# Kernel tuning notes

Hardware: AMD Instinct MI355X
Metric: run time of the kernel (lower is better)

Reference implementation:

```python
import jax, jax.numpy as jnp
import numpy as np

N_HEADS = 16


def setup_inputs() -> dict:
    key = jax.random.key(0)
    ks = jax.random.split(key, 9)
    B, S, D = 2, 2048, 1024
    s = 0.02
    return {
        "x": jax.random.normal(ks[0], (B, S, D), dtype=jnp.float32),
        "Wq": jax.random.normal(ks[1], (D, D), dtype=jnp.float32) * s,
        "bq": jax.random.normal(ks[2], (D,), dtype=jnp.float32) * s,
        "Wk": jax.random.normal(ks[3], (D, D), dtype=jnp.float32) * s,
        "bk": jax.random.normal(ks[4], (D,), dtype=jnp.float32) * s,
        "Wv": jax.random.normal(ks[5], (D, D), dtype=jnp.float32) * s,
        "bv": jax.random.normal(ks[6], (D,), dtype=jnp.float32) * s,
        "Wo": jax.random.normal(ks[7], (D, D), dtype=jnp.float32) * s,
        "bo": jax.random.normal(ks[8], (D,), dtype=jnp.float32) * s,
    }


def reference(x, Wq, bq, Wk, bk, Wv, bv, Wo, bo):
    B, S, D = x.shape
    H = N_HEADS
    hd = D // H
    # projections -> [B, H, S, hd]
    def heads(w, b):
        return (x @ w + b).reshape(B, S, H, hd).transpose(0, 2, 1, 3)
    Q, K, V = heads(Wq, bq), heads(Wk, bk), heads(Wv, bv)
    scores = jnp.einsum("bhqd,bhkd->bhqk", Q, K)
    causal = jnp.triu(jnp.ones((S, S), dtype=bool), k=1)  # True above diagonal
    scores = jnp.where(causal, -jnp.inf, scores)
    w = jax.nn.softmax(scores / jnp.sqrt(jnp.float32(hd)), axis=-1)
    ctx = jnp.einsum("bhqk,bhkd->bhqd", w, V).transpose(0, 2, 1, 3).reshape(B, S, D)
    return ctx @ Wo + bo
```

## Files before the change

kernel.cpp:

```cpp
#include <hip/hip_runtime.h>
#include <hip/hip_bf16.h>

typedef __attribute__((ext_vector_type(8))) short short8;
typedef __attribute__((ext_vector_type(4))) float floatx4;
typedef __attribute__((ext_vector_type(4))) int intx4;
typedef __attribute__((ext_vector_type(2))) int intx2;

#define D_MODEL 1024
#define SEQ     2048
#define NB      2
#define NH      16
#define HD      64
#define MROWS   4096
#define CZ      (0.125f * 1.44269504f)

__device__ __forceinline__ floatx4 mfma_bf16(short8 a, short8 b, floatx4 c) {
  return __builtin_amdgcn_mfma_f32_16x16x32_bf16(a, b, c, 0, 0, 0);
}

__device__ __forceinline__ void dma16(const __hip_bfloat16* g, __hip_bfloat16* l) {
  __builtin_amdgcn_global_load_lds(
      (const __attribute__((address_space(1))) void*)g,
      (__attribute__((address_space(3))) void*)l, 16, 0, 0);
}
#define WAIT_VM(n)  __asm__ __volatile__("s_waitcnt vmcnt(" #n ")" ::: "memory")
#define BARRIER()   __asm__ __volatile__("s_barrier" ::: "memory")
#define WAIT_LGKM() __asm__ __volatile__("s_waitcnt lgkmcnt(0)" ::: "memory")

__device__ __forceinline__ int pack2bf(float a, float b) {
  unsigned ua = __builtin_bit_cast(unsigned, a) + 0x8000u;
  unsigned ub = __builtin_bit_cast(unsigned, b) + 0x8000u;
  return (int)__builtin_amdgcn_perm(ub, ua, 0x07060302u);
}

__device__ __forceinline__ int cvtpk(float a, float b) {
  int r;
  __asm__("v_cvt_pk_bf16_f32 %0, %1, %2" : "=v"(r) : "v"(a), "v"(b));
  return r;
}

__global__ void prep_kernel(const float* __restrict__ x, __hip_bfloat16* __restrict__ xb,
                            const float* __restrict__ W0, const float* __restrict__ W1,
                            const float* __restrict__ W2, const float* __restrict__ W3,
                            __hip_bfloat16* __restrict__ T0, __hip_bfloat16* __restrict__ T1,
                            __hip_bfloat16* __restrict__ T2, __hip_bfloat16* __restrict__ T3) {
  const int z = blockIdx.z;
  if (z == 4) {
    const int tid = threadIdx.y * 32 + threadIdx.x;
    const int base = ((blockIdx.y * 32 + blockIdx.x) * 256 + tid) * 16;
#pragma unroll
    for (int c = 0; c < 4; c++) {
      float4 v = *(const float4*)(x + base + c * 4);
      __hip_bfloat16 tmp[4];
      tmp[0] = __float2bfloat16(v.x);
      tmp[1] = __float2bfloat16(v.y);
      tmp[2] = __float2bfloat16(v.z);
      tmp[3] = __float2bfloat16(v.w);
      *(ushort4*)(xb + base + c * 4) = *(ushort4*)tmp;
    }
    return;
  }
  const float* W = (z == 0) ? W0 : (z == 1) ? W1 : (z == 2) ? W2 : W3;
  __hip_bfloat16* Wt = (z == 0) ? T0 : (z == 1) ? T1 : (z == 2) ? T2 : T3;
  __shared__ float tile[32][33];
  int k0 = blockIdx.x * 32, n0 = blockIdx.y * 32;
  int tx = threadIdx.x, ty = threadIdx.y;
#pragma unroll
  for (int i = 0; i < 4; i++)
    tile[ty + 8 * i][tx] = W[(size_t)(k0 + ty + 8 * i) * D_MODEL + n0 + tx];
  __syncthreads();
#pragma unroll
  for (int i = 0; i < 4; i++)
    Wt[(size_t)(n0 + ty + 8 * i) * D_MODEL + k0 + tx] = __float2bfloat16(tile[tx][ty + 8 * i]);
}

template <int MODE>
__global__ __launch_bounds__(256) void gemm_kernel(
    const __hip_bfloat16* __restrict__ X,
    const __hip_bfloat16* __restrict__ Wt0, const __hip_bfloat16* __restrict__ Wt1,
    const __hip_bfloat16* __restrict__ Wt2,
    const float* __restrict__ b0, const float* __restrict__ b1, const float* __restrict__ b2,
    void* __restrict__ out0, void* __restrict__ out1, void* __restrict__ out2) {
  constexpr int MT = (MODE == 0) ? 128 : 64;
  constexpr int I = MT / 32;
  constexpr int NKT = D_MODEL / 32;
  constexpr int STAGE_BYTES = 3 * (MT * 32 + 128 * 32) * 2;
  constexpr int EPI_BYTES = 64 * 132 * 4;
  constexpr int SMEM_BYTES = (STAGE_BYTES > EPI_BYTES) ? STAGE_BYTES : EPI_BYTES;

  int n_idx, z, m_idx;
  if constexpr (MODE == 0) {
    const int lin = blockIdx.x + 8 * (blockIdx.y + 3 * blockIdx.z);
    n_idx = lin / 96;
    const int rem = lin - n_idx * 96;
    z = rem >> 5;
    m_idx = rem & 31;
  } else {
    const int lin = blockIdx.x + 8 * blockIdx.z;
    n_idx = lin >> 6;
    z = 0;
    m_idx = lin & 63;
  }

  const __hip_bfloat16* Wt = (z == 0) ? Wt0 : (z == 1) ? Wt1 : Wt2;
  const float* bias = (z == 0) ? b0 : (z == 1) ? b1 : b2;
  void* outp = (z == 0) ? out0 : (z == 1) ? out1 : out2;
  const float scale = (MODE == 0 && z == 0) ? CZ : 1.f;

  __shared__ __attribute__((aligned(16))) char smem[SMEM_BYTES];
  __hip_bfloat16* As = (__hip_bfloat16*)smem;
  __hip_bfloat16* Bs = (__hip_bfloat16*)smem + 3 * MT * 32;
  float* Es = (float*)smem;

  const int n0 = n_idx * 128;
  const int m0 = m_idx * MT;
  const int t = threadIdx.x;
  const int lane = t & 63, w = t >> 6;
  const int wm = (w >> 1) * (MT / 2), wn = (w & 1) * 64;
  const int lr = lane & 15;
  const int lq = lane >> 4;

  const __hip_bfloat16* Xp = X + (size_t)m0 * D_MODEL;
  const __hip_bfloat16* Wp = Wt + (size_t)n0 * D_MODEL;

  const int lrow = lane >> 2;
  const int skg = (((lane & 3) ^ ((lane >> 3) & 3)) << 3);
  const int srowA = ((MT == 128) ? (w << 5) : (w << 4)) + lrow;
  const int sbA0 = (((MT == 128) ? (w << 5) : (w << 4)) << 5);
  const int sbA1 = sbA0 + (16 << 5);
  const int srowB = (w << 5) + lrow;
  const int sbB0 = ((w << 5) << 5);
  const int sbB1 = sbB0 + (16 << 5);

#define STAGE_G(kt_, buf_)                                                              \
  {                                                                                     \
    const int kn_ = (kt_) * 32;                                                         \
    __hip_bfloat16* A_ = As + (buf_) * (MT * 32);                                       \
    __hip_bfloat16* B_ = Bs + (buf_) * (128 * 32);                                      \
    dma16(Xp + (size_t)srowA * D_MODEL + kn_ + skg, A_ + sbA0);                         \
    if (MT == 128) dma16(Xp + (size_t)(srowA + 16) * D_MODEL + kn_ + skg, A_ + sbA1);   \
    dma16(Wp + (size_t)srowB * D_MODEL + kn_ + skg, B_ + sbB0);                         \
    dma16(Wp + (size_t)(srowB + 16) * D_MODEL + kn_ + skg, B_ + sbB1);                  \
  }

  floatx4 acc[I][4];
#pragma unroll
  for (int i = 0; i < I; i++)
#pragma unroll
    for (int j = 0; j < 4; j++) acc[i][j] = (floatx4){0.f, 0.f, 0.f, 0.f};

  STAGE_G(0, 0);
  STAGE_G(1, 1);

  const int rcol = ((lq ^ ((lr >> 1) & 3)) << 3);

  int cb = 0;
  for (int kt = 0; kt < NKT; kt++) {
    if (kt < NKT - 1) {
      if constexpr (MODE == 0) WAIT_VM(4);
      else                     WAIT_VM(3);
    } else {
      WAIT_VM(0);
    }
    BARRIER();
    if (kt + 2 < NKT) {
      const int nb = (cb == 0) ? 2 : cb - 1;
      STAGE_G(kt + 2, nb);
    }
    const __hip_bfloat16* Ac = As + cb * (MT * 32);
    const __hip_bfloat16* Bc = Bs + cb * (128 * 32);
    short8 af[I], bfr[4];
#pragma unroll
    for (int i = 0; i < I; i++) af[i] = *(const short8*)&Ac[(wm + i * 16 + lr) * 32 + rcol];
#pragma unroll
    for (int j = 0; j < 4; j++) bfr[j] = *(const short8*)&Bc[(wn + j * 16 + lr) * 32 + rcol];
#pragma unroll
    for (int i = 0; i < I; i++)
#pragma unroll
      for (int j = 0; j < 4; j++) acc[i][j] = mfma_bf16(af[i], bfr[j], acc[i][j]);
    cb = (cb == 2) ? 0 : cb + 1;
  }
#undef STAGE_G

  float bvj[4];
#pragma unroll
  for (int j = 0; j < 4; j++) bvj[j] = bias[n0 + wn + j * 16 + lr];

  if constexpr (MODE == 1) {
    BARRIER();
#pragma unroll
    for (int i = 0; i < I; i++) {
      const int rowb = wm + i * 16 + lq * 4;
#pragma unroll
      for (int j = 0; j < 4; j++)
#pragma unroll
        for (int r = 0; r < 4; r++)
          Es[(rowb + r) * 132 + wn + j * 16 + lr] = acc[i][j][r] + bvj[j];
    }
    WAIT_LGKM();
    BARRIER();
    const int L = t >> 2, nseg = (t & 3) * 32;
    float* op = (float*)outp + (size_t)(m0 + L) * D_MODEL + n0 + nseg;
    const float* src = &Es[L * 132 + nseg];
#pragma unroll
    for (int k = 0; k < 8; k++) *(float4*)(op + 4 * k) = *(const float4*)(src + 4 * k);
  } else if (z != 2) {
    for (int c = 0; c < 2; c++) {
      BARRIER();
#pragma unroll
      for (int i2 = 0; i2 < 2; i2++) {
        const int i = 2 * c + i2;
        const int rowb = (w >> 1) * 32 + i2 * 16 + lq * 4;
#pragma unroll
        for (int j = 0; j < 4; j++)
#pragma unroll
          for (int r = 0; r < 4; r++)
            Es[(rowb + r) * 132 + wn + j * 16 + lr] = (acc[i][j][r] + bvj[j]) * scale;
      }
      WAIT_LGKM();
      BARRIER();
      const int L = t >> 2, nseg = (t & 3) * 32;
      const int m = m0 + ((L >> 5) << 6) + (c << 5) + (L & 31);
      const int bb = m >> 11, s = m & 2047;
      const int nn = n0 + nseg;
      __hip_bfloat16* op = (__hip_bfloat16*)outp +
          (((size_t)(bb * NH + (nn >> 6)) * SEQ + s) * HD + (nn & 63));
      const float* src = &Es[L * 132 + nseg];
#pragma unroll
      for (int k = 0; k < 4; k++) {
        intx4 pk;
        pk[0] = pack2bf(src[8 * k + 0], src[8 * k + 1]);
        pk[1] = pack2bf(src[8 * k + 2], src[8 * k + 3]);
        pk[2] = pack2bf(src[8 * k + 4], src[8 * k + 5]);
        pk[3] = pack2bf(src[8 * k + 6], src[8 * k + 7]);
        *(intx4*)(op + 8 * k) = pk;
      }
    }
  } else {
    for (int c = 0; c < 2; c++) {
      BARRIER();
#pragma unroll
      for (int j2 = 0; j2 < 2; j2++) {
        const int j = 2 * c + j2;
        const int nl = ((w & 1) << 5) + (j2 << 4) + lr;
#pragma unroll
        for (int i = 0; i < I; i++) {
          const int moff = (w >> 1) * 64 + i * 16 + lq * 4;
          floatx4 v = acc[i][j];
          v[0] += bvj[j]; v[1] += bvj[j]; v[2] += bvj[j]; v[3] += bvj[j];
          *(floatx4*)&Es[nl * 132 + moff] = v;
        }
      }
      WAIT_LGKM();
      BARRIER();
      const int nl = t >> 2, mseg = (t & 3) * 32;
      const int n = n0 + ((nl >> 5) << 6) + (c << 5) + (nl & 31);
      const int s0 = m0 & 2047, bb = m0 >> 11;
      __hip_bfloat16* op = (__hip_bfloat16*)outp +
          (((size_t)(bb * NH + (n >> 6)) * HD + (n & 63)) * SEQ + s0 + mseg);
      const float* src = &Es[nl * 132 + mseg];
#pragma unroll
      for (int k = 0; k < 4; k++) {
        intx4 pk;
        pk[0] = pack2bf(src[8 * k + 0], src[8 * k + 1]);
        pk[1] = pack2bf(src[8 * k + 2], src[8 * k + 3]);
        pk[2] = pack2bf(src[8 * k + 4], src[8 * k + 5]);
        pk[3] = pack2bf(src[8 * k + 6], src[8 * k + 7]);
        *(intx4*)(op + 8 * k) = pk;
      }
    }
  }
}

__global__ __launch_bounds__(256, 4) void attn_kernel(
    const __hip_bfloat16* __restrict__ Q, const __hip_bfloat16* __restrict__ Kg,
    const __hip_bfloat16* __restrict__ Vt, __hip_bfloat16* __restrict__ ctx) {
  const int bh = blockIdx.x;
  const int b = bh >> 4, h = bh & 15;
  const int qt = 31 - blockIdx.y;
  const int t = threadIdx.x, lane = t & 63, w = t >> 6;
  const int lr = lane & 15, lq = lane >> 4;
  const int wr = w & 1, wb = w >> 1;

  __shared__ __attribute__((aligned(16))) __hip_bfloat16 Ks[2][64 * 64];
  __shared__ __attribute__((aligned(16))) __hip_bfloat16 VTs[2][64 * 64];

  const __hip_bfloat16* Qb = Q + (size_t)bh * SEQ * HD;
  const __hip_bfloat16* Kb = Kg + (size_t)bh * SEQ * HD;
  const __hip_bfloat16* Vb = Vt + (size_t)bh * HD * SEQ;

  const int qrow0 = qt * 64 + wr * 32;

  short8 qf[2][2];
#pragma unroll
  for (int rt = 0; rt < 2; rt++)
#pragma unroll
    for (int ks = 0; ks < 2; ks++)
      qf[rt][ks] = *(const short8*)(Qb + (size_t)(qrow0 + rt * 16 + lr) * HD + ks * 32 + lq * 8);

  const int srow = (w << 4) + (lane >> 3);
  const int sgl = lane & 7;
  const int sb0 = (w << 4) << 6;
  const int sb1 = ((w << 4) + 8) << 6;

#define STAGE(tb, nb)                                                                  \
  {                                                                                    \
    const int r0 = srow, r1 = srow + 8;                                                \
    dma16(Kb + ((size_t)((tb) + r0) << 6) + ((sgl ^ (r0 & 7)) << 3), &Ks[nb][sb0]);    \
    dma16(Kb + ((size_t)((tb) + r1) << 6) + ((sgl ^ (r1 & 7)) << 3), &Ks[nb][sb1]);    \
    dma16(Vb + (size_t)r0 * SEQ + (tb) + ((sgl ^ (r0 & 7)) << 3), &VTs[nb][sb0]);      \
    dma16(Vb + (size_t)r1 * SEQ + (tb) + ((sgl ^ (r1 & 7)) << 3), &VTs[nb][sb1]);      \
  }

  const int nkt = qt + 1;
  STAGE(0, 0);

  floatx4 o[2][4];
#pragma unroll
  for (int rt = 0; rt < 2; rt++)
#pragma unroll
    for (int dt = 0; dt < 4; dt++) o[rt][dt] = (floatx4){0.f, 0.f, 0.f, 0.f};
  floatx4 lsacc[2];
  lsacc[0] = (floatx4){0.f, 0.f, 0.f, 0.f};
  lsacc[1] = (floatx4){0.f, 0.f, 0.f, 0.f};

  short8 ones;
#pragma unroll
  for (int j = 0; j < 8; j++) ones[j] = (short)0x3F80;

  const int kfb0 = ((wb << 4) + lr) << 6;
  const int kg0 = ((lq ^ (lr & 7)) << 3);
  const int kg1 = (((4 + lq) ^ (lr & 7)) << 3);
  const int vga = (((wb * 2 + (lq >> 1)) ^ (lr & 7)) << 3) + ((lq & 1) << 2);
  const int vgb = (((4 + wb * 2 + (lq >> 1)) ^ (lr & 7)) << 3) + ((lq & 1) << 2);

  for (int kt = 0; kt < nkt; kt++) {
    WAIT_VM(0);
    BARRIER();
    if (kt + 1 < nkt) STAGE((kt + 1) << 6, (kt + 1) & 1);

    const int kw0 = (kt << 6) + (wb << 4);
    if (kw0 <= qrow0 + 31) {
      const __hip_bfloat16* Kc = Ks[kt & 1];
      const __hip_bfloat16* Vc = VTs[kt & 1];

      short8 kf[2][2];
#pragma unroll
      for (int nt = 0; nt < 2; nt++) {
        kf[0][nt] = *(const short8*)&Kc[(nt << 11) + kfb0 + kg0];
        kf[1][nt] = *(const short8*)&Kc[(nt << 11) + kfb0 + kg1];
      }
      floatx4 s[2][2];
#pragma unroll
      for (int rt = 0; rt < 2; rt++)
#pragma unroll
        for (int nt = 0; nt < 2; nt++) s[rt][nt] = (floatx4){0.f, 0.f, 0.f, 0.f};
#pragma unroll
      for (int ks = 0; ks < 2; ks++)
#pragma unroll
        for (int nt = 0; nt < 2; nt++) {
          s[0][nt] = mfma_bf16(kf[ks][nt], qf[0][ks], s[0][nt]);
          s[1][nt] = mfma_bf16(kf[ks][nt], qf[1][ks], s[1][nt]);
        }

      const bool need_mask = (kw0 + 47 > qrow0);
      short8 pf[2];
#pragma unroll
      for (int rt = 0; rt < 2; rt++) {
        const int q = qrow0 + rt * 16 + lr;
        intx4 pk;
#pragma unroll
        for (int nt = 0; nt < 2; nt++) {
          const int kbase = (kt << 6) + (nt << 5) + (wb << 4) + (lq << 2);
          float x0 = s[rt][nt][0], x1 = s[rt][nt][1], x2 = s[rt][nt][2], x3 = s[rt][nt][3];
          if (need_mask) {
            x0 = (kbase + 0 <= q) ? x0 : -1e30f;
            x1 = (kbase + 1 <= q) ? x1 : -1e30f;
            x2 = (kbase + 2 <= q) ? x2 : -1e30f;
            x3 = (kbase + 3 <= q) ? x3 : -1e30f;
          }
          const float p0 = __builtin_amdgcn_exp2f(x0);
          const float p1 = __builtin_amdgcn_exp2f(x1);
          const float p2 = __builtin_amdgcn_exp2f(x2);
          const float p3 = __builtin_amdgcn_exp2f(x3);
          pk[2 * nt + 0] = cvtpk(p0, p1);
          pk[2 * nt + 1] = cvtpk(p2, p3);
        }
        pf[rt] = __builtin_bit_cast(short8, pk);
      }

      lsacc[0] = mfma_bf16(ones, pf[0], lsacc[0]);
      lsacc[1] = mfma_bf16(ones, pf[1], lsacc[1]);

#pragma unroll
      for (int dt = 0; dt < 4; dt++) {
        const int rb = ((dt << 4) + lr) << 6;
        intx4 vi;
        *(intx2*)&vi = *(const intx2*)&Vc[rb + vga];
        *(((intx2*)&vi) + 1) = *(const intx2*)&Vc[rb + vgb];
        short8 vf = __builtin_bit_cast(short8, vi);
        o[0][dt] = mfma_bf16(vf, pf[0], o[0][dt]);
        o[1][dt] = mfma_bf16(vf, pf[1], o[1][dt]);
      }
    }
  }

  BARRIER();
  if (wb == 1) {
    float* d0 = (float*)&Ks[0][0];
    float* d1 = (float*)&Ks[1][0];
    float* dl = (float*)&VTs[0][0];
    const int base = (wr << 10) + (lane << 4);
#pragma unroll
    for (int dt = 0; dt < 4; dt++) *(floatx4*)&d0[base + (dt << 2)] = o[0][dt];
#pragma unroll
    for (int dt = 0; dt < 4; dt++) *(floatx4*)&d1[base + (dt << 2)] = o[1][dt];
    dl[(wr << 7) + (lane << 1)] = lsacc[0][0];
    dl[(wr << 7) + (lane << 1) + 1] = lsacc[1][0];
    WAIT_LGKM();
  }
  BARRIER();
  if (wb == 0) {
    const float* d0 = (const float*)&Ks[0][0];
    const float* d1 = (const float*)&Ks[1][0];
    const float* dl = (const float*)&VTs[0][0];
    const int base = (wr << 10) + (lane << 4);
#pragma unroll
    for (int dt = 0; dt < 4; dt++) {
      o[0][dt] += *(const floatx4*)&d0[base + (dt << 2)];
      o[1][dt] += *(const floatx4*)&d1[base + (dt << 2)];
    }
    float inv[2];
    inv[0] = 1.f / (lsacc[0][0] + dl[(wr << 7) + (lane << 1)]);
    inv[1] = 1.f / (lsacc[1][0] + dl[(wr << 7) + (lane << 1) + 1]);
#pragma unroll
    for (int rt = 0; rt < 2; rt++) {
      const int row = qrow0 + rt * 16 + lr;
      __hip_bfloat16* cp = ctx + (size_t)b * SEQ * D_MODEL + (size_t)row * D_MODEL + h * HD;
#pragma unroll
      for (int dt = 0; dt < 4; dt++) {
        ushort4 pk;
        __hip_bfloat16* pp = (__hip_bfloat16*)&pk;
#pragma unroll
        for (int r = 0; r < 4; r++) pp[r] = __float2bfloat16(o[rt][dt][r] * inv[rt]);
        *(ushort4*)(cp + (dt << 4) + (lq << 2)) = pk;
      }
    }
  }
#undef STAGE
}

extern "C" void kernel_launch(void* const* d_in, const int* in_sizes, int n_in,
                              void* d_out, int out_size, void* d_ws, size_t ws_size,
                              hipStream_t stream) {
  const float* x  = (const float*)d_in[0];
  const float* Wq = (const float*)d_in[1];
  const float* bq = (const float*)d_in[2];
  const float* Wk = (const float*)d_in[3];
  const float* bk = (const float*)d_in[4];
  const float* Wv = (const float*)d_in[5];
  const float* bv = (const float*)d_in[6];
  const float* Wo = (const float*)d_in[7];
  const float* bo = (const float*)d_in[8];

  char* ws = (char*)d_ws;
  const size_t MB = 1u << 20;
  __hip_bfloat16* xb  = (__hip_bfloat16*)(ws + 0 * MB);
  __hip_bfloat16* wtq = (__hip_bfloat16*)(ws + 8 * MB);
  __hip_bfloat16* wtk = (__hip_bfloat16*)(ws + 10 * MB);
  __hip_bfloat16* wtv = (__hip_bfloat16*)(ws + 12 * MB);
  __hip_bfloat16* wto = (__hip_bfloat16*)(ws + 14 * MB);
  __hip_bfloat16* qb  = (__hip_bfloat16*)(ws + 16 * MB);
  __hip_bfloat16* kb  = (__hip_bfloat16*)(ws + 24 * MB);
  __hip_bfloat16* vt  = (__hip_bfloat16*)(ws + 32 * MB);
  __hip_bfloat16* ctx = xb;

  prep_kernel<<<dim3(32, 32, 5), dim3(32, 8), 0, stream>>>(x, xb, Wq, Wk, Wv, Wo,
                                                           wtq, wtk, wtv, wto);
  gemm_kernel<0><<<dim3(8, 3, 32), 256, 0, stream>>>(xb, wtq, wtk, wtv, bq, bk, bv,
                                                     (void*)qb, (void*)kb, (void*)vt);
  attn_kernel<<<dim3(32, 32), 256, 0, stream>>>(qb, kb, vt, ctx);
  gemm_kernel<1><<<dim3(8, 1, 64), 256, 0, stream>>>(ctx, wto, wto, wto, bo, bo, bo,
                                                     d_out, d_out, d_out);
}
```

Before: 188.0 us.

## Replace QKV projection GEMM with 256x256-tile, 512-thread double-buffered kernel

Adds a new QKV projection kernel that computes 256x256 output tiles with 8 waves, K-step 64, XOR-swizzled LDS, and double-buffered global-to-LDS DMA. Each load is split into quarters so the next tile's loads interleave with MFMA work, and s_setprio is raised around the MFMA blocks. The goal is more data reuse per loaded byte and fewer blocks than the 128x128 tiles. The trade-off is 128KB of LDS, only 192 blocks (fewer than the CU count), and more barriers per K step. The old MODE 0 code is removed from the templated GEMM, which now serves only the output projection.

Result: no change. 186.6 us (-0.7%).

```diff
diff --git a/kernel.cpp b/kernel.cpp
--- a/kernel.cpp
+++ b/kernel.cpp
@@ -72,6 +72,195 @@
 #pragma unroll
   for (int i = 0; i < 4; i++)
     Wt[(size_t)(n0 + ty + 8 * i) * D_MODEL + k0 + tx] = __float2bfloat16(tile[tx][ty + 8 * i]);
+}
+
+__global__ __launch_bounds__(512, 2) void gemm256_kernel(
+    const __hip_bfloat16* __restrict__ X,
+    const __hip_bfloat16* __restrict__ Wt0, const __hip_bfloat16* __restrict__ Wt1,
+    const __hip_bfloat16* __restrict__ Wt2,
+    const float* __restrict__ b0, const float* __restrict__ b1, const float* __restrict__ b2,
+    void* __restrict__ out0, void* __restrict__ out1, void* __restrict__ out2) {
+  constexpr int NKT = D_MODEL / 64;
+  constexpr int BUFE = 256 * 64;
+
+  const int z = blockIdx.y;
+  const __hip_bfloat16* Wt = (z == 0) ? Wt0 : (z == 1) ? Wt1 : Wt2;
+  const float* bias = (z == 0) ? b0 : (z == 1) ? b1 : b2;
+  void* outp = (z == 0) ? out0 : (z == 1) ? out1 : out2;
+  const float scale = (z == 0) ? CZ : 1.f;
+
+  __shared__ __attribute__((aligned(16))) char smem[131072];
+  __hip_bfloat16* As = (__hip_bfloat16*)smem;
+  __hip_bfloat16* Bs = (__hip_bfloat16*)smem + 2 * BUFE;
+  float* Es = (float*)smem;
+
+  const int n0 = blockIdx.x * 256;
+  const int m0 = blockIdx.z * 256;
+  const int t = threadIdx.x;
+  const int lane = t & 63, w = t >> 6;
+  const int wm = w >> 2, wn = w & 3;
+  const int lr = lane & 15, lq = lane >> 4;
+
+  const __hip_bfloat16* Xp = X + (size_t)m0 * D_MODEL;
+  const __hip_bfloat16* Wp = Wt + (size_t)n0 * D_MODEL;
+
+  const int srow = t >> 3;
+  const int sg = (t & 7) ^ (srow & 7);
+  const int wbase = (w << 3) << 6;
+
+#define STAGE_A8(kt_, u_)                                                             \
+  dma16(Xp + (size_t)(((u_) << 6) + srow) * D_MODEL + ((kt_) << 6) + (sg << 3),       \
+        As + (((kt_) & 1) ? BUFE : 0) + ((u_) << 12) + wbase)
+#define STAGE_B8(kt_, u_)                                                             \
+  dma16(Wp + (size_t)(((u_) << 6) + srow) * D_MODEL + ((kt_) << 6) + (sg << 3),       \
+        Bs + (((kt_) & 1) ? BUFE : 0) + ((u_) << 12) + wbase)
+
+  floatx4 acc[8][4];
+#pragma unroll
+  for (int i = 0; i < 8; i++)
+#pragma unroll
+    for (int j = 0; j < 4; j++) acc[i][j] = (floatx4){0.f, 0.f, 0.f, 0.f};
+
+  STAGE_B8(0, 0); STAGE_B8(0, 1); STAGE_B8(0, 2); STAGE_B8(0, 3);
+  STAGE_A8(0, 0); STAGE_A8(0, 2); STAGE_A8(0, 1); STAGE_A8(0, 3);
+
+#define READ_A2(dst, IB)                                                              \
+  _Pragma("unroll") for (int i2 = 0; i2 < 2; i2++) {                                  \
+    const int ra = (wm << 7) + (((IB) + i2) << 4) + lr;                               \
+    _Pragma("unroll") for (int ks = 0; ks < 2; ks++)                                  \
+      dst[i2][ks] = *(const short8*)&Ac[(ra << 6) + ((((ks << 2) + lq) ^ (ra & 7)) << 3)]; \
+  }
+#define MFMA_Q(IB, afr)                                                               \
+  __builtin_amdgcn_s_setprio(1);                                                      \
+  _Pragma("unroll") for (int i2 = 0; i2 < 2; i2++)                                    \
+  _Pragma("unroll") for (int j = 0; j < 4; j++) {                                     \
+    acc[(IB) + i2][j] = mfma_bf16(afr[i2][0], bf[j][0], acc[(IB) + i2][j]);           \
+    acc[(IB) + i2][j] = mfma_bf16(afr[i2][1], bf[j][1], acc[(IB) + i2][j]);           \
+  }                                                                                   \
+  __builtin_amdgcn_s_setprio(0);
+
+  for (int kt = 0; kt < NKT; kt++) {
+    const __hip_bfloat16* Ac = As + ((kt & 1) ? BUFE : 0);
+    const __hip_bfloat16* Bc = Bs + ((kt & 1) ? BUFE : 0);
+    const bool pre = (kt + 1 < NKT);
+
+    WAIT_VM(2);
+    BARRIER();
+    if (pre) { STAGE_B8(kt + 1, 0); STAGE_B8(kt + 1, 1); }
+    short8 bf[4][2];
+#pragma unroll
+    for (int j = 0; j < 4; j++) {
+      const int rb = (wn << 6) + (j << 4) + lr;
+#pragma unroll
+      for (int ks = 0; ks < 2; ks++)
+        bf[j][ks] = *(const short8*)&Bc[(rb << 6) + ((((ks << 2) + lq) ^ (rb & 7)) << 3)];
+    }
+    {
+      short8 a0[2][2];
+      READ_A2(a0, 0);
+      MFMA_Q(0, a0);
+    }
+    BARRIER();
+
+    if (pre) { STAGE_B8(kt + 1, 2); STAGE_B8(kt + 1, 3); }
+    {
+      short8 a1[2][2];
+      READ_A2(a1, 2);
+      MFMA_Q(2, a1);
+    }
+    BARRIER();
+
+    if (pre) { WAIT_VM(4); } else { WAIT_VM(0); }
+    BARRIER();
+    if (pre) { STAGE_A8(kt + 1, 0); STAGE_A8(kt + 1, 2); }
+    {
+      short8 a2[2][2];
+      READ_A2(a2, 4);
+      MFMA_Q(4, a2);
+    }
+    BARRIER();
+
+    if (pre) { STAGE_A8(kt + 1, 1); STAGE_A8(kt + 1, 3); }
+    {
+      short8 a3[2][2];
+      READ_A2(a3, 6);
+      MFMA_Q(6, a3);
+    }
+    BARRIER();
+  }
+#undef READ_A2
+#undef MFMA_Q
+#undef STAGE_A8
+#undef STAGE_B8
+
+  float bvj[4];
+#pragma unroll
+  for (int j = 0; j < 4; j++) bvj[j] = bias[n0 + (wn << 6) + j * 16 + lr];
+
+  if (z != 2) {
+    for (int c = 0; c < 4; c++) {
+      BARRIER();
+#pragma unroll
+      for (int i2 = 0; i2 < 2; i2++) {
+        const int rowl = (wm << 5) + (i2 << 4) + (lq << 2);
+#pragma unroll
+        for (int j = 0; j < 4; j++)
+#pragma unroll
+          for (int r = 0; r < 4; r++)
+            Es[(rowl + r) * 260 + (wn << 6) + j * 16 + lr] =
+                (acc[2 * c + i2][j][r] + bvj[j]) * scale;
+      }
+      WAIT_LGKM();
+      BARRIER();
+      const int rl = t >> 3, cs = (t & 7) * 32;
+      const int m = m0 + ((rl >> 5) << 7) + (c << 5) + (rl & 31);
+      const int bb = m >> 11, s = m & 2047;
+      const int n = n0 + cs;
+      __hip_bfloat16* op = (__hip_bfloat16*)outp +
+          (((size_t)(bb * NH + (n >> 6)) * SEQ + s) * HD + (n & 63));
+      const float* src = &Es[rl * 260 + cs];
+#pragma unroll
+      for (int k = 0; k < 4; k++) {
+        intx4 pk;
+        pk[0] = pack2bf(src[8 * k + 0], src[8 * k + 1]);
+        pk[1] = pack2bf(src[8 * k + 2], src[8 * k + 3]);
+        pk[2] = pack2bf(src[8 * k + 4], src[8 * k + 5]);
+        pk[3] = pack2bf(src[8 * k + 6], src[8 * k + 7]);
+        *(intx4*)(op + 8 * k) = pk;
+      }
+    }
+  } else {
+    for (int jj = 0; jj < 4; jj++) {
+      BARRIER();
+      {
+        const int nc = (wn << 4) + lr;
+#pragma unroll
+        for (int i = 0; i < 8; i++) {
+          const int ml = (wm << 7) + (i << 4) + (lq << 2);
+          floatx4 v = acc[i][jj];
+          v[0] += bvj[jj]; v[1] += bvj[jj]; v[2] += bvj[jj]; v[3] += bvj[jj];
+          *(floatx4*)&Es[nc * 260 + ml] = v;
+        }
+      }
+      WAIT_LGKM();
+      BARRIER();
+      const int nc2 = t >> 3, ms = (t & 7) * 32;
+      const int n = n0 + ((nc2 >> 4) << 6) + (jj << 4) + (nc2 & 15);
+      const int s0 = m0 & 2047, bb = m0 >> 11;
+      __hip_bfloat16* op = (__hip_bfloat16*)outp +
+          (((size_t)(bb * NH + (n >> 6)) * HD + (n & 63)) * SEQ + s0 + ms);
+      const float* src = &Es[nc2 * 260 + ms];
+#pragma unroll
+      for (int k = 0; k < 4; k++) {
+        intx4 pk;
+        pk[0] = pack2bf(src[8 * k + 0], src[8 * k + 1]);
+        pk[1] = pack2bf(src[8 * k + 2], src[8 * k + 3]);
+        pk[2] = pack2bf(src[8 * k + 4], src[8 * k + 5]);
+        pk[3] = pack2bf(src[8 * k + 6], src[8 * k + 7]);
+        *(intx4*)(op + 8 * k) = pk;
+      }
+    }
+  }
 }
 
 template <int MODE>
@@ -89,13 +278,7 @@
   constexpr int SMEM_BYTES = (STAGE_BYTES > EPI_BYTES) ? STAGE_BYTES : EPI_BYTES;
 
   int n_idx, z, m_idx;
-  if constexpr (MODE == 0) {
-    const int lin = blockIdx.x + 8 * (blockIdx.y + 3 * blockIdx.z);
-    n_idx = lin / 96;
-    const int rem = lin - n_idx * 96;
-    z = rem >> 5;
-    m_idx = rem & 31;
-  } else {
+  {
     const int lin = blockIdx.x + 8 * blockIdx.z;
     n_idx = lin >> 6;
     z = 0;
@@ -105,7 +288,6 @@
   const __hip_bfloat16* Wt = (z == 0) ? Wt0 : (z == 1) ? Wt1 : Wt2;
   const float* bias = (z == 0) ? b0 : (z == 1) ? b1 : b2;
   void* outp = (z == 0) ? out0 : (z == 1) ? out1 : out2;
-  const float scale = (MODE == 0 && z == 0) ? CZ : 1.f;
 
   __shared__ __attribute__((aligned(16))) char smem[SMEM_BYTES];
   __hip_bfloat16* As = (__hip_bfloat16*)smem;
@@ -157,8 +339,7 @@
   int cb = 0;
   for (int kt = 0; kt < NKT; kt++) {
     if (kt < NKT - 1) {
-      if constexpr (MODE == 0) WAIT_VM(4);
-      else                     WAIT_VM(3);
+      WAIT_VM(3);
     } else {
       WAIT_VM(0);
     }
@@ -186,90 +367,23 @@
 #pragma unroll
   for (int j = 0; j < 4; j++) bvj[j] = bias[n0 + wn + j * 16 + lr];
 
-  if constexpr (MODE == 1) {
-    BARRIER();
-#pragma unroll
-    for (int i = 0; i < I; i++) {
-      const int rowb = wm + i * 16 + lq * 4;
-#pragma unroll
-      for (int j = 0; j < 4; j++)
-#pragma unroll
-        for (int r = 0; r < 4; r++)
-          Es[(rowb + r) * 132 + wn + j * 16 + lr] = acc[i][j][r] + bvj[j];
-    }
-    WAIT_LGKM();
-    BARRIER();
-    const int L = t >> 2, nseg = (t & 3) * 32;
-    float* op = (float*)outp + (size_t)(m0 + L) * D_MODEL + n0 + nseg;
-    const float* src = &Es[L * 132 + nseg];
-#pragma unroll
-    for (int k = 0; k < 8; k++) *(float4*)(op + 4 * k) = *(const float4*)(src + 4 * k);
-  } else if (z != 2) {
-    for (int c = 0; c < 2; c++) {
-      BARRIER();
-#pragma unroll
-      for (int i2 = 0; i2 < 2; i2++) {
-        const int i = 2 * c + i2;
-        const int rowb = (w >> 1) * 32 + i2 * 16 + lq * 4;
-#pragma unroll
-        for (int j = 0; j < 4; j++)
-#pragma unroll
-          for (int r = 0; r < 4; r++)
-            Es[(rowb + r) * 132 + wn + j * 16 + lr] = (acc[i][j][r] + bvj[j]) * scale;
-      }
-      WAIT_LGKM();
-      BARRIER();
-      const int L = t >> 2, nseg = (t & 3) * 32;
-      const int m = m0 + ((L >> 5) << 6) + (c << 5) + (L & 31);
-      const int bb = m >> 11, s = m & 2047;
-      const int nn = n0 + nseg;
-      __hip_bfloat16* op = (__hip_bfloat16*)outp +
-          (((size_t)(bb * NH + (nn >> 6)) * SEQ + s) * HD + (nn & 63));
-      const float* src = &Es[L * 132 + nseg];
-#pragma unroll
-      for (int k = 0; k < 4; k++) {
-        intx4 pk;
-        pk[0] = pack2bf(src[8 * k + 0], src[8 * k + 1]);
-        pk[1] = pack2bf(src[8 * k + 2], src[8 * k + 3]);
-        pk[2] = pack2bf(src[8 * k + 4], src[8 * k + 5]);
-        pk[3] = pack2bf(src[8 * k + 6], src[8 * k + 7]);
-        *(intx4*)(op + 8 * k) = pk;
-      }
-    }
-  } else {
-    for (int c = 0; c < 2; c++) {
-      BARRIER();
-#pragma unroll
-      for (int j2 = 0; j2 < 2; j2++) {
-        const int j = 2 * c + j2;
-        const int nl = ((w & 1) << 5) + (j2 << 4) + lr;
-#pragma unroll
-        for (int i = 0; i < I; i++) {
-          const int moff = (w >> 1) * 64 + i * 16 + lq * 4;
-          floatx4 v = acc[i][j];
-          v[0] += bvj[j]; v[1] += bvj[j]; v[2] += bvj[j]; v[3] += bvj[j];
-          *(floatx4*)&Es[nl * 132 + moff] = v;
-        }
-      }
-      WAIT_LGKM();
-      BARRIER();
-      const int nl = t >> 2, mseg = (t & 3) * 32;
-      const int n = n0 + ((nl >> 5) << 6) + (c << 5) + (nl & 31);
-      const int s0 = m0 & 2047, bb = m0 >> 11;
-      __hip_bfloat16* op = (__hip_bfloat16*)outp +
-          (((size_t)(bb * NH + (n >> 6)) * HD + (n & 63)) * SEQ + s0 + mseg);
-      const float* src = &Es[nl * 132 + mseg];
-#pragma unroll
-      for (int k = 0; k < 4; k++) {
-        intx4 pk;
-        pk[0] = pack2bf(src[8 * k + 0], src[8 * k + 1]);
-        pk[1] = pack2bf(src[8 * k + 2], src[8 * k + 3]);
-        pk[2] = pack2bf(src[8 * k + 4], src[8 * k + 5]);
-        pk[3] = pack2bf(src[8 * k + 6], src[8 * k + 7]);
-        *(intx4*)(op + 8 * k) = pk;
-      }
-    }
-  }
+  BARRIER();
+#pragma unroll
+  for (int i = 0; i < I; i++) {
+    const int rowb = wm + i * 16 + lq * 4;
+#pragma unroll
+    for (int j = 0; j < 4; j++)
+#pragma unroll
+      for (int r = 0; r < 4; r++)
+        Es[(rowb + r) * 132 + wn + j * 16 + lr] = acc[i][j][r] + bvj[j];
+  }
+  WAIT_LGKM();
+  BARRIER();
+  const int L = t >> 2, nseg = (t & 3) * 32;
+  float* op = (float*)outp + (size_t)(m0 + L) * D_MODEL + n0 + nseg;
+  const float* src = &Es[L * 132 + nseg];
+#pragma unroll
+  for (int k = 0; k < 8; k++) *(float4*)(op + 4 * k) = *(const float4*)(src + 4 * k);
 }
 
 __global__ __launch_bounds__(256, 4) void attn_kernel(
@@ -477,7 +591,7 @@
 
   prep_kernel<<<dim3(32, 32, 5), dim3(32, 8), 0, stream>>>(x, xb, Wq, Wk, Wv, Wo,
                                                            wtq, wtk, wtv, wto);
-  gemm_kernel<0><<<dim3(8, 3, 32), 256, 0, stream>>>(xb, wtq, wtk, wtv, bq, bk, bv,
+  gemm256_kernel<<<dim3(4, 3, 16), 512, 0, stream>>>(xb, wtq, wtk, wtv, bq, bk, bv,
                                                      (void*)qb, (void*)kb, (void*)vt);
   attn_kernel<<<dim3(32, 32), 256, 0, stream>>>(qb, kb, vt, ctx);
   gemm_kernel<1><<<dim3(8, 1, 64), 256, 0, stream>>>(ctx, wto, wto, wto, bo, bo, bo,
```
